# Kernel tuning notes

Hardware: AMD Instinct MI355X
Metric: run time of the kernel (lower is better)

## Reference

```python
import jax, jax.numpy as jnp
import numpy as np

B, L, H, E = 4, 2048, 8, 64
NEG = -1e30  # stand-in for the repo's -3.4e38 overflow-to-inf masking trick


def setup_inputs() -> dict:
    key = jax.random.key(0)
    kq, kk, kv = jax.random.split(key, 3)
    return {
        "queries": jax.random.normal(kq, (B, L, H, E), dtype=jnp.float32),
        "keys": jax.random.normal(kk, (B, L, H, E), dtype=jnp.float32),
        "values": jax.random.normal(kv, (B, L, H, E), dtype=jnp.float32),
    }


def reference(queries, keys, values):
    b, l, h, e = queries.shape
    s = keys.shape[1]
    scale = 1.0 / np.sqrt(e).astype(np.float32)
    # [B,H,L,S] scores, materialized as in the original einsum
    scores = jnp.einsum('blhe,bshe->bhls', queries, keys)
    causal = jnp.tril(jnp.ones((l, s), dtype=bool))  # True = visible
    scores = jnp.where(causal, scores, NEG)
    A = jax.nn.softmax(scale * scores, axis=-1)  # dropout is identity at inference
    return jnp.einsum('bhls,bshd->blhd', A, values)
```

## Files before the change

### kernel.cpp

```cpp
#include <hip/hip_runtime.h>
#include <hip/hip_bf16.h>

namespace {

constexpr int B_ = 4, L = 2048, H = 8, E = 64;
constexpr int RS = H * E;
constexpr float CS = 0.125f * 1.44269504f;
constexpr float THR2 = 11.5f;

constexpr size_t ACCF = (size_t)2 * 32 * 8 * 128 * 64;
constexpr size_t MOFF = ACCF;
constexpr size_t PART_ROWS = (size_t)32 * 8 * 128;
constexpr size_t LOFF = MOFF + 2 * PART_ROWS;
constexpr size_t PART_FLOATS = LOFF + 2 * PART_ROWS;

typedef __attribute__((ext_vector_type(8))) short bf16x8;
typedef __attribute__((ext_vector_type(4))) float f32x4;

__device__ inline unsigned cvt2(float a, float b) {
  __hip_bfloat162 hh = __float22bfloat162_rn(make_float2(a, b));
  union { __hip_bfloat162 h; unsigned u; } c; c.h = hh; return c.u;
}

__global__ __launch_bounds__(512)
void fa_split(const float* __restrict__ Q, const float* __restrict__ K,
              const float* __restrict__ V, float* __restrict__ O,
              float* __restrict__ ws, int splitMode)
{
  const int tid  = (int)threadIdx.x;
  const int lane = tid & 63;
  const int wv   = tid >> 6;
  const int bi   = (int)blockIdx.x;
  const int bh   = bi & 31;
  const int pp   = (bi >> 5) & 7;
  const int role = splitMode ? (bi >> 8) : 2;
  const int b = bh >> 3, h = bh & 7;
  const int ln = lane & 15, lg = lane >> 4, d0 = lg * 4;

  int total, ph1sb0, qgA, k0A, qgB; bool finA, finB; int part;
  const int g = pp, v = 15 - pp;
  if (role == 0)      { total = 17; ph1sb0 = 2*g+2; qgA = g; k0A = 0;        finA = true;  qgB = v; finB = false; part = 0; }
  else if (role == 1) { total = 17; ph1sb0 = 1000;  qgA = v; k0A = 15 - 2*g; finA = false; qgB = 0; finB = false; part = 1; }
  else                { total = 34; ph1sb0 = 2*g+2; qgA = g; k0A = 0;        finA = true;  qgB = v; finB = true;  part = 0; }

  const size_t base = (size_t)b * L * RS + (size_t)h * E;
  const float* Qb = Q + base;
  const float* Kb = K + base;
  const float* Vb = V + base;
  float*       Ob = O + base;

  __shared__ __align__(16) unsigned char KT[2][64 * 128];
  __shared__ __align__(16) unsigned char VT[2][64 * 128];

  const int vdd = tid & 63, vc = tid >> 6;
  const int vkb = 4 * vc + ((vc >> 2) << 4);
  const int kky = tid >> 3, kc = tid & 7;
  float vr[8]; float4 kr0, kr1;
  const float* vp_it;
  const float* kp_it;

  auto stage_seek = [&](int ks) {
    const int kv0 = ks * 64;
    vp_it = Vb + (size_t)(kv0 + vkb) * RS + vdd;
    kp_it = Kb + (size_t)(kv0 + kky) * RS + 8 * kc;
  };
  auto stage_load = [&]() {
#pragma unroll
    for (int j = 0; j < 4; ++j) vr[j] = vp_it[(size_t)j * RS];
#pragma unroll
    for (int j = 0; j < 4; ++j) vr[4 + j] = vp_it[(size_t)(16 + j) * RS];
    kr0 = *(const float4*)kp_it; kr1 = *(const float4*)(kp_it + 4);
    vp_it += (size_t)64 * RS;
    kp_it += (size_t)64 * RS;
  };
  auto stage_write = [&](int bufI) {
    union { uint4 q; unsigned u[4]; } w;
    w.u[0] = cvt2(vr[0], vr[1]); w.u[1] = cvt2(vr[2], vr[3]);
    w.u[2] = cvt2(vr[4], vr[5]); w.u[3] = cvt2(vr[6], vr[7]);
    *(uint4*)(VT[bufI] + vdd * 128 + 16 * (vc ^ (vdd & 7))) = w.q;
    union { uint4 q; unsigned u[4]; } y;
    y.u[0] = cvt2(kr0.x, kr0.y); y.u[1] = cvt2(kr0.z, kr0.w);
    y.u[2] = cvt2(kr1.x, kr1.y); y.u[3] = cvt2(kr1.z, kr1.w);
    *(uint4*)(KT[bufI] + kky * 128 + 16 * (kc ^ (kky & 7))) = y.q;
  };

  int qg = qgA; bool curFin = finA;
  int qrow0 = qg * 128 + wv * 16;
  int nsW   = (qrow0 + 79) >> 6;

  bf16x8 qf0, qf1;
  auto load_q = [&]() {
    const float* qp = Qb + (size_t)(qrow0 + ln) * RS + 8 * lg;
    float4 a = *(const float4*)qp,        c = *(const float4*)(qp + 4);
    float4 d = *(const float4*)(qp + 32), e = *(const float4*)(qp + 36);
    union { bf16x8 v8; unsigned u[4]; } r0, r1;
    r0.u[0] = cvt2(a.x * CS, a.y * CS); r0.u[1] = cvt2(a.z * CS, a.w * CS);
    r0.u[2] = cvt2(c.x * CS, c.y * CS); r0.u[3] = cvt2(c.z * CS, c.w * CS);
    r1.u[0] = cvt2(d.x * CS, d.y * CS); r1.u[1] = cvt2(d.z * CS, d.w * CS);
    r1.u[2] = cvt2(e.x * CS, e.y * CS); r1.u[3] = cvt2(e.z * CS, e.w * CS);
    qf0 = r0.v8; qf1 = r1.v8;
  };
  load_q();

  union { bf16x8 v8; unsigned u[4]; } ones;
#pragma unroll
  for (int j = 0; j < 4; ++j) ones.u[j] = 0x3F803F80u;

  f32x4 acc[4], acc4;
#pragma unroll
  for (int nt = 0; nt < 4; ++nt) acc[nt] = (f32x4){0.f, 0.f, 0.f, 0.f};
  acc4 = (f32x4){0.f, 0.f, 0.f, 0.f};
  float m = -1e30f;

  auto epilogue = [&]() {
    if (curFin) {
#pragma unroll
      for (int r = 0; r < 4; ++r) {
        const float il = 1.0f / acc4[r];
#pragma unroll
        for (int nt = 0; nt < 4; ++nt)
          Ob[(size_t)(qrow0 + d0 + r) * RS + (ln + 16 * nt)] = acc[nt][r] * il;
      }
    } else {
      const int vg = qg - 8;
      const size_t rb = ((size_t)part * 32 + bh) * 1024 + (size_t)vg * 128;
#pragma unroll
      for (int nt = 0; nt < 4; ++nt)
#pragma unroll
        for (int r = 0; r < 4; ++r)
          ws[(rb + wv * 16 + d0 + r) * 64 + ln + 16 * nt] = acc[nt][r];
      if (lane < 16) ws[MOFF + rb + wv * 16 + lane] = m;
      if (ln == 0) {
#pragma unroll
        for (int r = 0; r < 4; ++r)
          ws[LOFF + rb + wv * 16 + d0 + r] = acc4[r];
      }
    }
  };

  stage_seek(k0A);
  stage_load();
  stage_write(0);
  __syncthreads();
  int buf = 0;

  for (int sb = 0; sb < total; ++sb) {
    const bool haveNext = (sb + 1) < total;
    if (haveNext) {
      if (sb + 1 == ph1sb0) stage_seek(0);
      stage_load();
    }
    const int kstep = (sb < ph1sb0) ? (k0A + sb) : (sb - ph1sb0);

    if (kstep < nsW) {
      __builtin_amdgcn_s_setprio(1);
      const unsigned char* Kt = KT[buf];
      const int swzr = 16 * (ln & 7);

      f32x4 st[4];
#pragma unroll
      for (int kt = 0; kt < 4; ++kt) {
        const unsigned char* kr = Kt + (16 * kt + ln) * 128;
        const bf16x8 kfa = *(const bf16x8*)(kr + ((16 * lg) ^ swzr));
        const bf16x8 kfb = *(const bf16x8*)(kr + ((16 * lg + 64) ^ swzr));
        f32x4 s = (f32x4){0.f, 0.f, 0.f, 0.f};
        s = __builtin_amdgcn_mfma_f32_16x16x32_bf16(kfa, qf0, s, 0, 0, 0);
        s = __builtin_amdgcn_mfma_f32_16x16x32_bf16(kfb, qf1, s, 0, 0, 0);
        st[kt] = s;
      }

      float x[16];
#pragma unroll
      for (int kt = 0; kt < 4; ++kt)
#pragma unroll
        for (int r = 0; r < 4; ++r) x[4 * kt + r] = st[kt][r];

      if (kstep == nsW - 1) {
        const int kv0 = kstep * 64;
        const int qr = qrow0 + ln;
#pragma unroll
        for (int kt = 0; kt < 4; ++kt)
#pragma unroll
          for (int r = 0; r < 4; ++r) {
            const int key = kv0 + 16 * kt + d0 + r;
            if (key > qr) x[4 * kt + r] = -1e30f;
          }
      }

      float t8[8];
#pragma unroll
      for (int e = 0; e < 8; ++e) t8[e] = fmaxf(x[e], x[8 + e]);
      float t4a = fmaxf(t8[0], t8[4]), t4b = fmaxf(t8[1], t8[5]);
      float t4c = fmaxf(t8[2], t8[6]), t4d = fmaxf(t8[3], t8[7]);
      float mx = fmaxf(fmaxf(t4a, t4b), fmaxf(t4c, t4d));

      if (!__all(mx <= m + THR2)) {
        float gm = fmaxf(mx, __shfl_xor(mx, 16, 64));
        gm = fmaxf(gm, __shfl_xor(gm, 32, 64));
        const float newm = fmaxf(m, gm);
        const float sc = __builtin_exp2f(m - newm);
        float scr[4];
#pragma unroll
        for (int r = 0; r < 4; ++r) scr[r] = __shfl(sc, d0 + r, 64);
#pragma unroll
        for (int nt = 0; nt < 4; ++nt) {
          acc[nt][0] *= scr[0]; acc[nt][1] *= scr[1];
          acc[nt][2] *= scr[2]; acc[nt][3] *= scr[3];
        }
        acc4[0] *= scr[0]; acc4[1] *= scr[1];
        acc4[2] *= scr[2]; acc4[3] *= scr[3];
        m = newm;
      }

      float p[16];
#pragma unroll
      for (int e = 0; e < 16; ++e) p[e] = __builtin_exp2f(x[e] - m);

      const unsigned char* Vt = VT[buf];
#pragma unroll
      for (int kg = 0; kg < 2; ++kg) {
        union { bf16x8 v8; unsigned u[4]; } pf;
#pragma unroll
        for (int j = 0; j < 4; ++j)
          pf.u[j] = cvt2(p[8 * kg + 2 * j], p[8 * kg + 2 * j + 1]);
#pragma unroll
        for (int nt = 0; nt < 4; ++nt) {
          const int row = ln + 16 * nt;
          const bf16x8 vf = *(const bf16x8*)(
              Vt + row * 128 + 16 * ((lg + 4 * kg) ^ (ln & 7)));
          acc[nt] = __builtin_amdgcn_mfma_f32_16x16x32_bf16(pf.v8, vf, acc[nt], 0, 0, 0);
        }
        acc4 = __builtin_amdgcn_mfma_f32_16x16x32_bf16(pf.v8, ones.v8, acc4, 0, 0, 0);
      }
      __builtin_amdgcn_s_setprio(0);
    }

    if (sb == ph1sb0 - 1) {
      epilogue();
#pragma unroll
      for (int nt = 0; nt < 4; ++nt) acc[nt] = (f32x4){0.f, 0.f, 0.f, 0.f};
      acc4 = (f32x4){0.f, 0.f, 0.f, 0.f};
      m = -1e30f;
      qg = qgB; curFin = finB;
      qrow0 = qg * 128 + wv * 16;
      nsW = (qrow0 + 79) >> 6;
      load_q();
    }

    if (haveNext) stage_write(buf ^ 1);
    __syncthreads();
    buf ^= 1;
  }

  epilogue();
}

__global__ __launch_bounds__(256)
void fa_merge(const float* __restrict__ ws, float* __restrict__ O)
{
  const int idx = (int)blockIdx.x * 256 + (int)threadIdx.x;
  const int d4  = idx & 15;
  const int row = (idx >> 4) & 127;
  const int vg  = (idx >> 11) & 7;
  const int bh  = idx >> 14;
  const size_t rbase = ((size_t)bh * 8 + vg) * 128 + row;

  const float m0 = ws[MOFF + rbase],             l0 = ws[LOFF + rbase];
  const float m1 = ws[MOFF + PART_ROWS + rbase], l1 = ws[LOFF + PART_ROWS + rbase];
  const float M  = fmaxf(m0, m1);
  const float e0 = __builtin_exp2f(m0 - M), e1 = __builtin_exp2f(m1 - M);
  const float inv = 1.0f / (l0 * e0 + l1 * e1);

  const float4 a0 = *(const float4*)(ws + rbase * 64 + 4 * d4);
  const float4 a1 = *(const float4*)(ws + PART_ROWS * 64 + rbase * 64 + 4 * d4);

  const int b = bh >> 3, h = bh & 7;
  const int orow = (8 + vg) * 128 + row;
  float4 o;
  o.x = (a0.x * e0 + a1.x * e1) * inv;
  o.y = (a0.y * e0 + a1.y * e1) * inv;
  o.z = (a0.z * e0 + a1.z * e1) * inv;
  o.w = (a0.w * e0 + a1.w * e1) * inv;
  *(float4*)(O + ((size_t)(b * L + orow) * H + h) * E + 4 * d4) = o;
}

}

extern "C" void kernel_launch(void* const* d_in, const int* in_sizes, int n_in,
                              void* d_out, int out_size, void* d_ws, size_t ws_size,
                              hipStream_t stream) {
  const float* Q = (const float*)d_in[0];
  const float* K = (const float*)d_in[1];
  const float* V = (const float*)d_in[2];
  float* O = (float*)d_out;
  (void)in_sizes; (void)n_in; (void)out_size;

  const bool split = ws_size >= PART_FLOATS * sizeof(float);
  if (split) {
    fa_split<<<512, 512, 0, stream>>>(Q, K, V, O, (float*)d_ws, 1);
    fa_merge<<<2048, 256, 0, stream>>>((const float*)d_ws, O);
  } else {
    fa_split<<<256, 512, 0, stream>>>(Q, K, V, O, (float*)d_ws, 0);
  }
}
```

Baseline: 49.91 us.

## Process two KV tiles per barrier using four-slot LDS ring buffer

Doubles the K/V shared-memory staging to four buffers, so each loop iteration computes two KV steps between barriers and writes the next pair into the other half. This halves the number of __syncthreads calls in the attention main loop and cuts the stall that comes with each barrier. In exchange LDS use doubles to 64KB per block, which may reduce occupancy. The control flow also becomes more complex around the phase switch and odd step counts.

```diff
diff --git a/kernel.cpp b/kernel.cpp
--- a/kernel.cpp
+++ b/kernel.cpp
@@ -49,8 +49,8 @@
   const float* Vb = V + base;
   float*       Ob = O + base;
 
-  __shared__ __align__(16) unsigned char KT[2][64 * 128];
-  __shared__ __align__(16) unsigned char VT[2][64 * 128];
+  __shared__ __align__(16) unsigned char KT[4][64 * 128];
+  __shared__ __align__(16) unsigned char VT[4][64 * 128];
 
   const int vdd = tid & 63, vc = tid >> 6;
   const int vkb = 4 * vc + ((vc >> 2) << 4);
@@ -138,23 +138,10 @@
     }
   };
 
-  stage_seek(k0A);
-  stage_load();
-  stage_write(0);
-  __syncthreads();
-  int buf = 0;
-
-  for (int sb = 0; sb < total; ++sb) {
-    const bool haveNext = (sb + 1) < total;
-    if (haveNext) {
-      if (sb + 1 == ph1sb0) stage_seek(0);
-      stage_load();
-    }
-    const int kstep = (sb < ph1sb0) ? (k0A + sb) : (sb - ph1sb0);
-
+  auto compute = [&](int kstep, int bufI) {
     if (kstep < nsW) {
       __builtin_amdgcn_s_setprio(1);
-      const unsigned char* Kt = KT[buf];
+      const unsigned char* Kt = KT[bufI];
       const int swzr = 16 * (ln & 7);
 
       f32x4 st[4];
@@ -216,7 +203,7 @@
 #pragma unroll
       for (int e = 0; e < 16; ++e) p[e] = __builtin_exp2f(x[e] - m);
 
-      const unsigned char* Vt = VT[buf];
+      const unsigned char* Vt = VT[bufI];
 #pragma unroll
       for (int kg = 0; kg < 2; ++kg) {
         union { bf16x8 v8; unsigned u[4]; } pf;
@@ -234,7 +221,9 @@
       }
       __builtin_amdgcn_s_setprio(0);
     }
-
+  };
+
+  auto phase_switch = [&](int sb) {
     if (sb == ph1sb0 - 1) {
       epilogue();
 #pragma unroll
@@ -246,10 +235,43 @@
       nsW = (qrow0 + 79) >> 6;
       load_q();
     }
-
-    if (haveNext) stage_write(buf ^ 1);
+  };
+
+  auto kstep_of = [&](int sb) { return (sb < ph1sb0) ? (k0A + sb) : (sb - ph1sb0); };
+
+  stage_seek(k0A);
+  stage_load(); stage_write(0);
+  stage_load(); stage_write(1);
+  __syncthreads();
+
+  int bp = 0, sb = 0;
+  while (sb + 1 < total) {
+    const int r0 = 2 * bp, r1 = r0 + 1;
+    const int w0 = 2 * (bp ^ 1), w1 = w0 + 1;
+
+    if (sb + 2 < total) {
+      if (sb + 2 == ph1sb0) stage_seek(0);
+      stage_load();
+    }
+    compute(kstep_of(sb), r0);
+    phase_switch(sb);
+    if (sb + 2 < total) stage_write(w0);
+
+    if (sb + 3 < total) {
+      if (sb + 3 == ph1sb0) stage_seek(0);
+      stage_load();
+    }
+    compute(kstep_of(sb + 1), r1);
+    phase_switch(sb + 1);
+    if (sb + 3 < total) stage_write(w1);
+
     __syncthreads();
-    buf ^= 1;
+    bp ^= 1;
+    sb += 2;
+  }
+  if (sb < total) {
+    compute(kstep_of(sb), 2 * bp);
+    phase_switch(sb);
   }
 
   epilogue();
```

Measured after the change: 52.55 us. 5.3% more time.
